# Kernel optimization log

Hardware: AMD Instinct MI355X
Metric: run time of the kernel (lower is better)

The kernel has to match this reference:

```python
import jax, jax.numpy as jnp
import numpy as np
import math

B, L, S, D = 4, 4096, 4096, 256
EPS = 1e-5

def _layernorm(x, g, b):
    mu = jnp.mean(x, axis=-1, keepdims=True)
    var = jnp.mean(jnp.square(x - mu), axis=-1, keepdims=True)
    return (x - mu) * jax.lax.rsqrt(var + EPS) * g + b

def setup_inputs() -> dict:
    key = jax.random.key(0)
    ks = jax.random.split(key, 14)
    s = 1.0 / math.sqrt(D)
    s2 = 1.0 / math.sqrt(2 * D)
    inp = {
        "source": jax.random.normal(ks[0], (B, L, D), jnp.float32),
        "target": jax.random.normal(ks[1], (B, S, D), jnp.float32),
        # linear weights stored as [in, out]
        "Wq": jax.random.uniform(ks[2], (D, D), jnp.float32, -s, s),
        "bq": jnp.zeros((D,), jnp.float32),
        "Wk": jax.random.uniform(ks[3], (D, D), jnp.float32, -s, s),
        "bk": jnp.zeros((D,), jnp.float32),
        "Wv": jax.random.uniform(ks[4], (D, D), jnp.float32, -s, s),
        "bv": jnp.zeros((D,), jnp.float32),
        "Wm": jax.random.uniform(ks[5], (D, D), jnp.float32, -s, s),
        "bm": jnp.zeros((D,), jnp.float32),
        "g1": jnp.ones((D,), jnp.float32),
        "beta1": jnp.zeros((D,), jnp.float32),
        "W1": jax.random.uniform(ks[6], (2 * D, 2 * D), jnp.float32, -s2, s2),
        "W2": jax.random.uniform(ks[7], (2 * D, D), jnp.float32, -s2, s2),
        "g2": jnp.ones((D,), jnp.float32),
        "beta2": jnp.zeros((D,), jnp.float32),
    }
    return inp

def reference(source, target, Wq, bq, Wk, bk, Wv, bv, Wm, bm, g1, beta1, W1, W2, g2, beta2):
    q = source @ Wq + bq              # [B, L, D]
    k = target @ Wk + bk              # [B, S, D]
    v = target @ Wv + bv              # [B, S, D]
    scale = 1.0 / math.sqrt(D)
    scores = jnp.einsum("bld,bsd->bls", q, k) * scale   # [B, L, S] materialized, as in source
    attn = jax.nn.softmax(scores, axis=-1)
    message = jnp.einsum("bls,bsd->bld", attn, v)        # [B, L, D]
    message = message @ Wm + bm
    message = _layernorm(message, g1, beta1)
    h = jnp.concatenate([source, message], axis=-1)      # [B, L, 2D]
    h = jax.nn.gelu(h @ W1, approximate=False)           # torch GELU is exact erf
    message = _layernorm(h @ W2, g2, beta2)
    return source + message
```

## Files before the change

### kernel.cpp

```cpp
#include <hip/hip_runtime.h>

typedef __bf16 bf16x8 __attribute__((ext_vector_type(8)));
typedef float f32x16 __attribute__((ext_vector_type(16)));
typedef float f32x4 __attribute__((ext_vector_type(4)));
typedef unsigned int u32;
typedef unsigned int u32x4 __attribute__((ext_vector_type(4)));
typedef unsigned short u16;
typedef unsigned short u16x4 __attribute__((ext_vector_type(4)));
typedef unsigned short u16x8 __attribute__((ext_vector_type(8)));

#define DEV static __device__ __forceinline__
#define AS1 __attribute__((address_space(1)))
#define AS3 __attribute__((address_space(3)))

DEV u16 f2bf(float f){
  unsigned u = __float_as_uint(f);
  u += 0x7FFFu + ((u >> 16) & 1u);
  return (u16)(u >> 16);
}
DEV float bf2f(u16 h){ return __uint_as_float(((u32)h) << 16); }

DEV void stage16(const u16* gsrc, const u16* ldst){
  __builtin_amdgcn_global_load_lds((const AS1 u32*)(unsigned long long)gsrc,
                                   (AS3 u32*)(u32)(unsigned long long)ldst,
                                   16, 0, 0);
}

constexpr int BATCH = 4, LQ = 4096, SK = 4096, DH = 256, BL = BATCH * LQ;
constexpr int NHALF = 2;
constexpr int ITERS = SK / NHALF / 64;

__global__ void prep_weights(const float* __restrict__ Wq, const float* __restrict__ Wk,
                             const float* __restrict__ Wv, const float* __restrict__ Wm,
                             const float* __restrict__ W1, const float* __restrict__ W2,
                             const float* __restrict__ bk, const float* __restrict__ bv,
                             u16* __restrict__ WqT, u16* __restrict__ WkvT,
                             u16* __restrict__ WmT,
                             u16* __restrict__ W1T, u16* __restrict__ W2T,
                             float* __restrict__ bkv){
  int idx = blockIdx.x * 256 + threadIdx.x;
  if (idx < 262144){
    int which = idx >> 16, i2 = idx & 65535;
    int r = i2 >> 8, c = i2 & 255;
    const float* S = (which==0)?Wq:(which==1)?Wk:(which==2)?Wv:Wm;
    u16*         D = (which==0)?WqT:(which==1)?WkvT:(which==2)?(WkvT+65536):WmT;
    D[c*256 + r] = f2bf(S[i2]);
  } else if (idx < 524288){
    int i2 = idx - 262144;
    int r = i2 >> 9, c = i2 & 511;
    W1T[c*512 + r] = f2bf(W1[i2]);
  } else if (idx < 655360){
    int i2 = idx - 524288;
    int r = i2 >> 8, c = i2 & 255;
    W2T[(size_t)c*512 + r] = f2bf(W2[i2]);
  } else if (idx < 655872){
    int i2 = idx - 655360;
    bkv[i2] = (i2 < 256) ? bk[i2] : bv[i2 - 256];
  }
}

__global__ __launch_bounds__(512, 2) void qkv_gemm(
  const float* __restrict__ src, const float* __restrict__ tgt,
  const u16* __restrict__ WqT, const u16* __restrict__ WkvT,
  const float* __restrict__ bq, const float* __restrict__ bkv,
  u16* __restrict__ qbuf, u16* __restrict__ kbuf, u16* __restrict__ vtbuf,
  u16* __restrict__ hcat, float qscale)
{
  __shared__ u16 A_lds[64 * 64];
  __shared__ u16 B_lds[256 * 64];
  const int tid = threadIdx.x, lane = tid & 63, wid = tid >> 6;
  const int ql = lane & 31, g = lane >> 5;
  const int path = blockIdx.x;
  const int m0 = blockIdx.y * 64;
  const float* Af = (path == 0) ? src : tgt;
  const u16* BTp = (path == 0) ? WqT : (WkvT + (size_t)(path - 1) * 65536);
  const float* bias = (path == 0) ? bq : (bkv + (path - 1) * 256);
  const int ar = tid >> 3, ac = (tid & 7) * 8;

  f32x16 acc[2] = {};
  f32x4 af0, af1;
  u32x4 breg[4];

#define QKV_LOAD_A(kb) do { \
    af0 = *(const f32x4*)&Af[(size_t)(m0+ar)*256 + (kb)*64 + ac]; \
    af1 = *(const f32x4*)&Af[(size_t)(m0+ar)*256 + (kb)*64 + ac + 4]; \
  } while(0)
#define QKV_LOAD_B(kb) do { \
    _Pragma("unroll") \
    for (int i = 0; i < 4; i++){ int item = tid + i*512; int r = item>>3, c = (item&7)*8; \
      breg[i] = *(const u32x4*)&BTp[(size_t)r*256 + (kb)*64 + c]; } \
  } while(0)

  QKV_LOAD_A(0); QKV_LOAD_B(0);

  for (int kb = 0; kb < 4; ++kb){
    __syncthreads();
    { u16x8 h;
      h[0]=f2bf(af0[0]); h[1]=f2bf(af0[1]); h[2]=f2bf(af0[2]); h[3]=f2bf(af0[3]);
      h[4]=f2bf(af1[0]); h[5]=f2bf(af1[1]); h[6]=f2bf(af1[2]); h[7]=f2bf(af1[3]);
      *(u16x8*)&A_lds[ar*64 + (ac ^ ((ar&7)*8))] = h;
      if (path == 0) *(u16x8*)&hcat[(size_t)(m0+ar)*512 + kb*64 + ac] = h;
    }
    #pragma unroll
    for (int i = 0; i < 4; i++){ int item = tid + i*512; int r = item>>3, c = (item&7)*8;
      *(u32x4*)&B_lds[r*64 + (c ^ ((r&7)*8))] = breg[i]; }
    __syncthreads();
    if (kb + 1 < 4){ QKV_LOAD_A(kb+1); QKV_LOAD_B(kb+1); }

    #pragma unroll
    for (int kk = 0; kk < 4; kk++){
      bf16x8 af[2];
      #pragma unroll
      for (int mi = 0; mi < 2; mi++)
        af[mi] = __builtin_bit_cast(bf16x8,
          *(const u32x4*)&A_lds[(mi*32+ql)*64 + ((kk*16+g*8) ^ ((ql&7)*8))]);
      bf16x8 bf = __builtin_bit_cast(bf16x8,
        *(const u32x4*)&B_lds[(wid*32+ql)*64 + ((kk*16+g*8) ^ ((ql&7)*8))]);
      #pragma unroll
      for (int mi = 0; mi < 2; mi++)
        acc[mi] = __builtin_amdgcn_mfma_f32_32x32x16_bf16(af[mi], bf, acc[mi], 0, 0, 0);
    }
  }

  const int col = wid*32 + ql;
  const float bv = bias[col];
  if (path == 2){
    #pragma unroll
    for (int mi = 0; mi < 2; mi++)
      #pragma unroll
      for (int qd = 0; qd < 4; qd++){
        u16x4 h;
        #pragma unroll
        for (int i = 0; i < 4; i++) h[i] = f2bf(acc[mi][qd*4+i] + bv);
        int row0 = m0 + mi*32 + qd*8 + 4*g;
        int bb = row0 >> 12, ss = row0 & 4095;
        *(u16x4*)&vtbuf[((size_t)bb*DH + col)*SK + ss] = h;
      }
  } else {
    u16* outp = (path == 0) ? qbuf : kbuf;
    const float sc = (path == 0) ? qscale : 1.0f;
    #pragma unroll
    for (int mi = 0; mi < 2; mi++)
      #pragma unroll
      for (int j = 0; j < 16; j++){
        int row = m0 + mi*32 + (j&3) + 8*(j>>2) + 4*g;
        outp[(size_t)row*256 + col] = f2bf((acc[mi][j] + bv) * sc);
      }
  }
}

__global__ __launch_bounds__(512, 2) void gemm_ln_wm(
  const u16* __restrict__ opart, const float* __restrict__ stats,
  const u16* __restrict__ BTp, const float* __restrict__ bias,
  const float* __restrict__ gamma, const float* __restrict__ beta,
  u16* __restrict__ outp)
{
  __shared__ __align__(16) char smem[65792];
  u16* A_lds = (u16*)smem;
  u16* B_lds = (u16*)(smem + 8192);
  float* scratch = (float*)smem;

  const int tid = threadIdx.x, lane = tid & 63, wid = tid >> 6;
  const int ql = lane & 31, g = lane >> 5;
  const int m0 = blockIdx.x * 64;
  const int ar = tid >> 3, ac = (tid & 7) * 8;

  float winv;
  { int row = m0 + ar;
    winv = 1.f / (stats[row] + stats[(size_t)BL + row]); }

  f32x16 acc[2] = {};
  u32x4 areg, areg2;
  u32x4 breg[4];

#define WM_LOAD_A(kb) do { \
    areg  = *(const u32x4*)&opart[(size_t)(m0+ar)*DH + (kb)*64 + ac]; \
    areg2 = *(const u32x4*)&opart[(size_t)BL*DH + (size_t)(m0+ar)*DH + (kb)*64 + ac]; \
  } while(0)
#define WM_LOAD_B(kb) do { \
    _Pragma("unroll") \
    for (int i = 0; i < 4; i++){ int item = tid + i*512; int r = item>>3, c = (item&7)*8; \
      breg[i] = *(const u32x4*)&BTp[(size_t)r*256 + (kb)*64 + c]; } \
  } while(0)

  WM_LOAD_A(0); WM_LOAD_B(0);

  for (int kb = 0; kb < 4; ++kb){
    __syncthreads();
    { u16x8 h;
      #pragma unroll
      for (int e = 0; e < 8; e++){
        u16 h0 = (u16)(areg[e>>1]  >> ((e&1)*16));
        u16 h1 = (u16)(areg2[e>>1] >> ((e&1)*16));
        h[e] = f2bf((bf2f(h0) + bf2f(h1)) * winv);
      }
      *(u16x8*)&A_lds[ar*64 + (ac ^ ((ar&7)*8))] = h; }
    #pragma unroll
    for (int i = 0; i < 4; i++){ int item = tid + i*512; int r = item>>3, c = (item&7)*8;
      *(u32x4*)&B_lds[r*64 + (c ^ ((r&7)*8))] = breg[i]; }
    __syncthreads();
    if (kb + 1 < 4){ WM_LOAD_A(kb+1); WM_LOAD_B(kb+1); }

    #pragma unroll
    for (int kk = 0; kk < 4; kk++){
      bf16x8 af[2];
      #pragma unroll
      for (int mi = 0; mi < 2; mi++)
        af[mi] = __builtin_bit_cast(bf16x8,
          *(const u32x4*)&A_lds[(mi*32+ql)*64 + ((kk*16+g*8) ^ ((ql&7)*8))]);
      bf16x8 bf = __builtin_bit_cast(bf16x8,
        *(const u32x4*)&B_lds[(wid*32+ql)*64 + ((kk*16+g*8) ^ ((ql&7)*8))]);
      #pragma unroll
      for (int mi = 0; mi < 2; mi++)
        acc[mi] = __builtin_amdgcn_mfma_f32_32x32x16_bf16(af[mi], bf, acc[mi], 0, 0, 0);
    }
  }

  __syncthreads();

  const float bv = bias[wid*32 + ql];
  #pragma unroll
  for (int mi = 0; mi < 2; mi++)
    #pragma unroll
    for (int j = 0; j < 16; j++){
      int row = mi*32 + (j&3) + 8*(j>>2) + 4*g;
      scratch[row*257 + wid*32 + ql] = acc[mi][j] + bv;
    }
  __syncthreads();

  f32x4 gv = *(const f32x4*)&gamma[lane*4];
  f32x4 bvv = *(const f32x4*)&beta[lane*4];
  #pragma unroll
  for (int rr = 0; rr < 8; rr++){
    const int row = wid*8 + rr;
    f32x4 v = *(const f32x4*)&scratch[row*257 + lane*4];
    float s1 = v[0]+v[1]+v[2]+v[3];
    float s2 = v[0]*v[0]+v[1]*v[1]+v[2]*v[2]+v[3]*v[3];
    #pragma unroll
    for (int m = 1; m < 64; m <<= 1){ s1 += __shfl_xor(s1, m, 64); s2 += __shfl_xor(s2, m, 64); }
    float mu = s1 * (1.f/DH);
    float var = s2 * (1.f/DH) - mu*mu;
    float rstd = rsqrtf(var + 1e-5f);
    u16x4 h;
    #pragma unroll
    for (int i = 0; i < 4; i++) h[i] = f2bf((v[i]-mu)*rstd*gv[i] + bvv[i]);
    *(u16x4*)&outp[(size_t)(m0+row)*512 + 256 + lane*4] = h;
  }
}

__global__ __launch_bounds__(512, 2) void fused_mlp(
  const u16* __restrict__ hcat, const u16* __restrict__ W1T,
  const u16* __restrict__ W2T, const float* __restrict__ gamma,
  const float* __restrict__ beta, const float* __restrict__ src,
  float* __restrict__ outp)
{
  __shared__ __align__(16) char smem[98304];
  u16* A1 = (u16*)smem;
  u16* B1 = (u16*)(smem + 8192);
  u16* Hl = (u16*)smem;
  u16* B2 = (u16*)(smem + 65536);
  float* scratch = (float*)smem;

  const int tid = threadIdx.x, lane = tid & 63, wid = tid >> 6;
  const int ql = lane & 31, g = lane >> 5;
  const int m0 = blockIdx.x * 64;

  f32x16 acc1[2][2] = {};
  for (int kb = 0; kb < 8; ++kb){
    if (kb) __syncthreads();
    { int r = tid >> 3, slot = tid & 7;
      stage16(&hcat[(size_t)(m0+r)*512 + kb*64 + ((slot ^ (r&7))<<3)],
              &A1[tid*8]); }
    #pragma unroll
    for (int i = 0; i < 8; i++){
      int grp = tid + i*512; int r = grp>>3, slot = grp&7;
      stage16(&W1T[(size_t)r*512 + kb*64 + ((slot ^ (r&7))<<3)], &B1[grp*8]);
    }
    __syncthreads();
    #pragma unroll
    for (int kk = 0; kk < 4; kk++){
      bf16x8 af[2];
      #pragma unroll
      for (int mi = 0; mi < 2; mi++)
        af[mi] = __builtin_bit_cast(bf16x8,
          *(const u32x4*)&A1[(mi*32+ql)*64 + ((kk*16+g*8) ^ ((ql&7)*8))]);
      #pragma unroll
      for (int ni = 0; ni < 2; ni++){
        int rB = wid*64 + ni*32 + ql;
        bf16x8 bf = __builtin_bit_cast(bf16x8,
          *(const u32x4*)&B1[rB*64 + ((kk*16+g*8) ^ ((ql&7)*8))]);
        #pragma unroll
        for (int mi = 0; mi < 2; mi++)
          acc1[mi][ni] = __builtin_amdgcn_mfma_f32_32x32x16_bf16(af[mi], bf, acc1[mi][ni], 0, 0, 0);
      }
    }
  }
  __syncthreads();

  #pragma unroll
  for (int mi = 0; mi < 2; mi++)
    #pragma unroll
    for (int ni = 0; ni < 2; ni++){
      const int col = wid*64 + ni*32 + ql;
      const int s = col >> 3;
      #pragma unroll
      for (int j = 0; j < 16; j++){
        int row = mi*32 + (j&3) + 8*(j>>2) + 4*g;
        float v = acc1[mi][ni][j];
        v = 0.5f * v * (1.f + erff(v * 0.70710678118f));
        Hl[row*512 + ((s ^ (row&7))<<3) + (col&7)] = f2bf(v);
      }
    }
  __syncthreads();

  f32x16 acc2[2] = {};
  for (int kb = 0; kb < 8; ++kb){
    if (kb) __syncthreads();
    #pragma unroll
    for (int i = 0; i < 4; i++){
      int grp = tid + i*512; int r = grp>>3, slot = grp&7;
      stage16(&W2T[(size_t)r*512 + kb*64 + ((slot ^ (r&7))<<3)], &B2[grp*8]);
    }
    __syncthreads();
    #pragma unroll
    for (int kk = 0; kk < 4; kk++){
      int c0s = (kb*64 + kk*16 + g*8) >> 3;
      bf16x8 af[2];
      #pragma unroll
      for (int mi = 0; mi < 2; mi++){
        int row = mi*32 + ql;
        af[mi] = __builtin_bit_cast(bf16x8,
          *(const u32x4*)&Hl[row*512 + ((c0s ^ (row&7))<<3)]);
      }
      bf16x8 bf = __builtin_bit_cast(bf16x8,
        *(const u32x4*)&B2[(wid*32+ql)*64 + ((kk*16+g*8) ^ ((ql&7)*8))]);
      #pragma unroll
      for (int mi = 0; mi < 2; mi++)
        acc2[mi] = __builtin_amdgcn_mfma_f32_32x32x16_bf16(af[mi], bf, acc2[mi], 0, 0, 0);
    }
  }
  __syncthreads();

  #pragma unroll
  for (int mi = 0; mi < 2; mi++)
    #pragma unroll
    for (int j = 0; j < 16; j++){
      int row = mi*32 + (j&3) + 8*(j>>2) + 4*g;
      scratch[row*257 + wid*32 + ql] = acc2[mi][j];
    }
  __syncthreads();

  f32x4 gv = *(const f32x4*)&gamma[lane*4];
  f32x4 bvv = *(const f32x4*)&beta[lane*4];
  #pragma unroll
  for (int rr = 0; rr < 8; rr++){
    const int row = wid*8 + rr;
    f32x4 v = *(const f32x4*)&scratch[row*257 + lane*4];
    float s1 = v[0]+v[1]+v[2]+v[3];
    float s2 = v[0]*v[0]+v[1]*v[1]+v[2]*v[2]+v[3]*v[3];
    #pragma unroll
    for (int m = 1; m < 64; m <<= 1){ s1 += __shfl_xor(s1, m, 64); s2 += __shfl_xor(s2, m, 64); }
    float mu = s1 * (1.f/DH);
    float var = s2 * (1.f/DH) - mu*mu;
    float rstd = rsqrtf(var + 1e-5f);
    f32x4 s = *(const f32x4*)&src[(size_t)(m0+row)*DH + lane*4];
    f32x4 o;
    #pragma unroll
    for (int i = 0; i < 4; i++) o[i] = s[i] + (v[i]-mu)*rstd*gv[i] + bvv[i];
    *(f32x4*)&outp[(size_t)(m0+row)*DH + lane*4] = o;
  }
}

__global__ __launch_bounds__(512, 2) void attn_kernel(
  const u16* __restrict__ qb, const u16* __restrict__ kb,
  const u16* __restrict__ vtb, u16* __restrict__ opart, float* __restrict__ stats)
{
  __shared__ u16 K_lds[2][64 * 256];
  __shared__ u16 VT_lds[2][256 * 64];
  __shared__ u32x4 P_exch[4][4][64];
  __shared__ float L_exch[4][2][32];

  const int tid = threadIdx.x;
  const int wid = tid >> 6, lane = tid & 63;
  const int ql = lane & 31, g = lane >> 5;
  const int qpair = wid >> 1, sh = wid & 1;
  const int b = blockIdx.y, half = blockIdx.z;
  const int qrow0 = blockIdx.x * 128 + qpair * 32;
  const int s0base = half * (SK / NHALF);

  const u16* kbase = kb  + (size_t)b * SK * DH;
  const u16* vbase = vtb + (size_t)b * DH * SK;

#define STAGE_K(bi, s0) do { \
    _Pragma("unroll") \
    for (int i = 0; i < 4; i++){ \
      int grp = tid + i*512; int s = grp>>5, slot = grp&31; \
      stage16(kbase + (size_t)((s0)+s)*DH + ((slot ^ (s&31))<<3), \
              &K_lds[bi][(i*512 + wid*64)*8]); \
    } } while(0)
#define STAGE_V(bi, s0) do { \
    _Pragma("unroll") \
    for (int i = 0; i < 4; i++){ \
      int grp = tid + i*512; int d = grp>>3, slot = grp&7; \
      stage16(vbase + (size_t)d*SK + (s0) + ((slot ^ (d&7))<<3), \
              &VT_lds[bi][(i*512 + wid*64)*8]); \
    } } while(0)

  STAGE_K(0, s0base);
  STAGE_V(0, s0base);

  bf16x8 qf[16];
  {
    const u16* qp = qb + ((size_t)(b*LQ + qrow0 + ql)) * DH + g * 8;
    #pragma unroll
    for (int kk = 0; kk < 16; kk++)
      qf[kk] = __builtin_bit_cast(bf16x8, *(const u32x4*)(qp + kk*16));
  }

  f32x16 accO[4] = {};
  float l_lane = 0.f;

  __syncthreads();

  for (int it = 0; it < ITERS; ++it){
    const int cur = it & 1;
    if (it + 1 < ITERS){
      STAGE_K(cur ^ 1, s0base + (it+1)*64);
      STAGE_V(cur ^ 1, s0base + (it+1)*64);
    }

    f32x16 ps = {};
    __builtin_amdgcn_s_setprio(1);
    #pragma unroll
    for (int kk = 0; kk < 16; ++kk){
      bf16x8 kf = __builtin_bit_cast(bf16x8,
        *(const u32x4*)&K_lds[cur][(sh*32+ql)*256 + (((kk*2+g) ^ ql)<<3)]);
      ps = __builtin_amdgcn_mfma_f32_32x32x16_bf16(kf, qf[kk], ps, 0, 0, 0);
    }
    __builtin_amdgcn_s_setprio(0);

    #pragma unroll
    for (int j = 0; j < 16; j++) ps[j] = exp2f(ps[j]);

    u32 Wp[4][2];
    #pragma unroll
    for (int qd = 0; qd < 4; qd++)
      #pragma unroll
      for (int h = 0; h < 2; h++){
        float lo = ps[qd*4 + 2*h], hi = ps[qd*4 + 2*h + 1];
        asm("v_cvt_pk_bf16_f32 %0, %1, %2" : "=v"(Wp[qd][h]) : "v"(lo), "v"(hi));
      }
    bf16x8 pfo[2];
    #pragma unroll
    for (int i = 0; i < 2; i++){
      const int qp2 = i * 2;
      u32 a0 = Wp[qp2][0], b0 = Wp[qp2+1][0];
      u32 a1 = Wp[qp2][1], b1 = Wp[qp2+1][1];
      asm("v_permlane32_swap_b32 %0, %1" : "+v"(a0), "+v"(b0));
      asm("v_permlane32_swap_b32 %0, %1" : "+v"(a1), "+v"(b1));
      u32x4 w; w[0] = a0; w[1] = a1; w[2] = b0; w[3] = b1;
      P_exch[qpair][sh*2 + i][lane] = w;
      pfo[i] = __builtin_bit_cast(bf16x8, w);
    }

    __builtin_amdgcn_s_setprio(1);
    #pragma unroll
    for (int dt = 0; dt < 4; dt++){
      const int dtg = sh*4 + dt;
      const int k0 = sh*2;
      bf16x8 vf0 = __builtin_bit_cast(bf16x8,
        *(const u32x4*)&VT_lds[cur][(dtg*32+ql)*64 + ((((k0+0)*2+g) ^ (ql&7))<<3)]);
      accO[dt] = __builtin_amdgcn_mfma_f32_32x32x16_bf16(vf0, pfo[0], accO[dt], 0, 0, 0);
      bf16x8 vf1 = __builtin_bit_cast(bf16x8,
        *(const u32x4*)&VT_lds[cur][(dtg*32+ql)*64 + ((((k0+1)*2+g) ^ (ql&7))<<3)]);
      accO[dt] = __builtin_amdgcn_mfma_f32_32x32x16_bf16(vf1, pfo[1], accO[dt], 0, 0, 0);
    }
    __builtin_amdgcn_s_setprio(0);

    { float s8[8];
      #pragma unroll
      for (int j = 0; j < 8; j++) s8[j] = ps[j] + ps[j+8];
      l_lane += ((s8[0]+s8[4]) + (s8[1]+s8[5])) + ((s8[2]+s8[6]) + (s8[3]+s8[7])); }

    asm volatile("s_waitcnt lgkmcnt(0)" ::: "memory");
    __builtin_amdgcn_s_barrier();
    __builtin_amdgcn_sched_barrier(0);

    bf16x8 pfp0 = __builtin_bit_cast(bf16x8, P_exch[qpair][(sh^1)*2 + 0][lane]);
    bf16x8 pfp1 = __builtin_bit_cast(bf16x8, P_exch[qpair][(sh^1)*2 + 1][lane]);

    __builtin_amdgcn_s_setprio(1);
    #pragma unroll
    for (int dt = 0; dt < 4; dt++){
      const int dtg = sh*4 + dt;
      const int k0 = (sh^1)*2;
      bf16x8 vf0 = __builtin_bit_cast(bf16x8,
        *(const u32x4*)&VT_lds[cur][(dtg*32+ql)*64 + ((((k0+0)*2+g) ^ (ql&7))<<3)]);
      accO[dt] = __builtin_amdgcn_mfma_f32_32x32x16_bf16(vf0, pfp0, accO[dt], 0, 0, 0);
      bf16x8 vf1 = __builtin_bit_cast(bf16x8,
        *(const u32x4*)&VT_lds[cur][(dtg*32+ql)*64 + ((((k0+1)*2+g) ^ (ql&7))<<3)]);
      accO[dt] = __builtin_amdgcn_mfma_f32_32x32x16_bf16(vf1, pfp1, accO[dt], 0, 0, 0);
    }
    __builtin_amdgcn_s_setprio(0);

    asm volatile("s_waitcnt vmcnt(0) lgkmcnt(0)" ::: "memory");
    __builtin_amdgcn_s_barrier();
    __builtin_amdgcn_sched_barrier(0);
  }

  float l_run = l_lane + __shfl_xor(l_lane, 32, 64);
  if (g == 0) L_exch[qpair][sh][ql] = l_run;
  __syncthreads();
  float l_tot = l_run + L_exch[qpair][sh^1][ql];

  const int rowb = b * LQ + qrow0;
  if (sh == 0 && g == 0)
    stats[(size_t)half*BL + rowb + ql] = l_tot;

  float* scratch = (float*)&K_lds[0][0] + wid * 1056;
  #pragma unroll
  for (int dt = 0; dt < 4; dt++){
    const int dtg = sh*4 + dt;
    #pragma unroll
    for (int j = 0; j < 16; j++){
      int dl = (j&3) + 8*(j>>2) + 4*g;
      scratch[ql*33 + dl] = accO[dt][j];
    }
    int q2 = lane >> 1, dl2 = (lane & 1) * 16;
    u16x8 h0, h1;
    #pragma unroll
    for (int i = 0; i < 8; i++){ h0[i] = f2bf(scratch[q2*33 + dl2 + i]);
                                 h1[i] = f2bf(scratch[q2*33 + dl2 + 8 + i]); }
    u16* op = &opart[((size_t)half*BL + rowb + q2)*DH + dtg*32 + dl2];
    *(u16x8*)op = h0;
    *(u16x8*)(op + 8) = h1;
  }
}

extern "C" void kernel_launch(void* const* d_in, const int* in_sizes, int n_in,
                              void* d_out, int out_size, void* d_ws, size_t ws_size,
                              hipStream_t stream)
{
  const float* source = (const float*)d_in[0];
  const float* target = (const float*)d_in[1];
  const float* Wq = (const float*)d_in[2];  const float* bq = (const float*)d_in[3];
  const float* Wk = (const float*)d_in[4];  const float* bk = (const float*)d_in[5];
  const float* Wv = (const float*)d_in[6];  const float* bv = (const float*)d_in[7];
  const float* Wm = (const float*)d_in[8];  const float* bm = (const float*)d_in[9];
  const float* g1 = (const float*)d_in[10]; const float* be1 = (const float*)d_in[11];
  const float* W1 = (const float*)d_in[12]; const float* W2 = (const float*)d_in[13];
  const float* g2 = (const float*)d_in[14]; const float* be2 = (const float*)d_in[15];

  char* ws = (char*)d_ws;
  u16* WqT  = (u16*)(ws);
  u16* WkvT = (u16*)(ws + (size_t)(1u<<17));
  u16* WmT  = (u16*)(ws + (size_t)3*(1u<<17));
  u16* W1T  = (u16*)(ws + (size_t)4*(1u<<17));
  u16* W2T  = (u16*)(ws + (size_t)8*(1u<<17));
  float* bkv = (float*)(ws + (size_t)10*(1u<<17));
  size_t off = (size_t)10*(1u<<17) + 4096;
  u16* qbuf  = (u16*)(ws + off); off += (size_t)BL*DH*2;
  u16* kbuf  = (u16*)(ws + off); off += (size_t)BL*DH*2;
  u16* vtbuf = (u16*)(ws + off); off += (size_t)BL*DH*2;
  u16* hcat  = (u16*)(ws + off); off += (size_t)BL*512*2;
  u16* opart = (u16*)(ws + off); off += (size_t)NHALF*BL*DH*2;
  float* stats = (float*)(ws + off); off += (size_t)NHALF*BL*4;

  prep_weights<<<dim3(2562), 256, 0, stream>>>(Wq, Wk, Wv, Wm, W1, W2, bk, bv,
                                               WqT, WkvT, WmT, W1T, W2T, bkv);

  const float qscale = 1.4426950408889634f / 16.0f;
  qkv_gemm<<<dim3(3, BL/64), 512, 0, stream>>>(
      source, target, WqT, WkvT, bq, bkv, qbuf, kbuf, vtbuf, hcat, qscale);

  attn_kernel<<<dim3(LQ/128, BATCH, NHALF), 512, 0, stream>>>(qbuf, kbuf, vtbuf, opart, stats);

  gemm_ln_wm<<<dim3(BL/64), 512, 0, stream>>>(opart, stats, WmT, bm, g1, be1, hcat);

  fused_mlp<<<dim3(BL/64), 512, 0, stream>>>(hcat, W1T, W2T, g2, be2, source,
                                             (float*)d_out);
}
```

Before: 153.0 us.

## Fuse Wm projection+LayerNorm with MLP kernel, keeping concat tile in LDS

Merges the Wm GEMM/LayerNorm kernel and the MLP kernel into one kernel that builds the [source, message] bf16 tile in shared memory, converting source directly from fp32. This removes the global hcat buffer, its writes from the QKV kernel and its reads in the MLP, plus one kernel launch. It raises shared memory per block to about 128 KB, which limits residency to one block per CU.

```diff
diff --git a/kernel.cpp b/kernel.cpp
--- a/kernel.cpp
+++ b/kernel.cpp
@@ -64,7 +64,7 @@
   const u16* __restrict__ WqT, const u16* __restrict__ WkvT,
   const float* __restrict__ bq, const float* __restrict__ bkv,
   u16* __restrict__ qbuf, u16* __restrict__ kbuf, u16* __restrict__ vtbuf,
-  u16* __restrict__ hcat, float qscale)
+  float qscale)
 {
   __shared__ u16 A_lds[64 * 64];
   __shared__ u16 B_lds[256 * 64];
@@ -99,7 +99,6 @@
       h[0]=f2bf(af0[0]); h[1]=f2bf(af0[1]); h[2]=f2bf(af0[2]); h[3]=f2bf(af0[3]);
       h[4]=f2bf(af1[0]); h[5]=f2bf(af1[1]); h[6]=f2bf(af1[2]); h[7]=f2bf(af1[3]);
       *(u16x8*)&A_lds[ar*64 + (ac ^ ((ar&7)*8))] = h;
-      if (path == 0) *(u16x8*)&hcat[(size_t)(m0+ar)*512 + kb*64 + ac] = h;
     }
     #pragma unroll
     for (int i = 0; i < 4; i++){ int item = tid + i*512; int r = item>>3, c = (item&7)*8;
@@ -149,21 +148,40 @@
   }
 }
 
-__global__ __launch_bounds__(512, 2) void gemm_ln_wm(
+__global__ __launch_bounds__(512, 2) void wm_mlp(
   const u16* __restrict__ opart, const float* __restrict__ stats,
-  const u16* __restrict__ BTp, const float* __restrict__ bias,
-  const float* __restrict__ gamma, const float* __restrict__ beta,
-  u16* __restrict__ outp)
+  const u16* __restrict__ WmT, const float* __restrict__ bm,
+  const float* __restrict__ g1, const float* __restrict__ be1,
+  const u16* __restrict__ W1T, const u16* __restrict__ W2T,
+  const float* __restrict__ g2, const float* __restrict__ be2,
+  const float* __restrict__ src, float* __restrict__ outp)
 {
-  __shared__ __align__(16) char smem[65792];
-  u16* A_lds = (u16*)smem;
-  u16* B_lds = (u16*)(smem + 8192);
-  float* scratch = (float*)smem;
+  __shared__ __align__(16) char smem[131328];
+  u16* Hc = (u16*)smem;
+  char* rb = smem + 65536;
+  u16* A_lds = (u16*)rb;
+  u16* B_lds = (u16*)(rb + 8192);
+  float* scr = (float*)rb;
+  u16* B1 = (u16*)rb;
+  u16* B2 = (u16*)rb;
 
   const int tid = threadIdx.x, lane = tid & 63, wid = tid >> 6;
   const int ql = lane & 31, g = lane >> 5;
   const int m0 = blockIdx.x * 64;
   const int ar = tid >> 3, ac = (tid & 7) * 8;
+
+  #pragma unroll
+  for (int i = 0; i < 4; i++){
+    int idx = tid + i*512;
+    int r = idx >> 5, c8 = (idx & 31) * 8;
+    f32x4 a = *(const f32x4*)&src[(size_t)(m0+r)*256 + c8];
+    f32x4 b = *(const f32x4*)&src[(size_t)(m0+r)*256 + c8 + 4];
+    u16x8 h;
+    h[0]=f2bf(a[0]); h[1]=f2bf(a[1]); h[2]=f2bf(a[2]); h[3]=f2bf(a[3]);
+    h[4]=f2bf(b[0]); h[5]=f2bf(b[1]); h[6]=f2bf(b[2]); h[7]=f2bf(b[3]);
+    int s = c8 >> 3;
+    *(u16x8*)&Hc[r*512 + ((s ^ (r&7))<<3)] = h;
+  }
 
   float winv;
   { int row = m0 + ar;
@@ -180,9 +198,10 @@
 #define WM_LOAD_B(kb) do { \
     _Pragma("unroll") \
     for (int i = 0; i < 4; i++){ int item = tid + i*512; int r = item>>3, c = (item&7)*8; \
-      breg[i] = *(const u32x4*)&BTp[(size_t)r*256 + (kb)*64 + c]; } \
+      breg[i] = *(const u32x4*)&BTpWm[(size_t)r*256 + (kb)*64 + c]; } \
   } while(0)
 
+  const u16* BTpWm = WmT;
   WM_LOAD_A(0); WM_LOAD_B(0);
 
   for (int kb = 0; kb < 4; ++kb){
@@ -218,59 +237,43 @@
 
   __syncthreads();
 
-  const float bv = bias[wid*32 + ql];
-  #pragma unroll
-  for (int mi = 0; mi < 2; mi++)
-    #pragma unroll
-    for (int j = 0; j < 16; j++){
-      int row = mi*32 + (j&3) + 8*(j>>2) + 4*g;
-      scratch[row*257 + wid*32 + ql] = acc[mi][j] + bv;
-    }
-  __syncthreads();
-
-  f32x4 gv = *(const f32x4*)&gamma[lane*4];
-  f32x4 bvv = *(const f32x4*)&beta[lane*4];
-  #pragma unroll
-  for (int rr = 0; rr < 8; rr++){
-    const int row = wid*8 + rr;
-    f32x4 v = *(const f32x4*)&scratch[row*257 + lane*4];
-    float s1 = v[0]+v[1]+v[2]+v[3];
-    float s2 = v[0]*v[0]+v[1]*v[1]+v[2]*v[2]+v[3]*v[3];
-    #pragma unroll
-    for (int m = 1; m < 64; m <<= 1){ s1 += __shfl_xor(s1, m, 64); s2 += __shfl_xor(s2, m, 64); }
-    float mu = s1 * (1.f/DH);
-    float var = s2 * (1.f/DH) - mu*mu;
-    float rstd = rsqrtf(var + 1e-5f);
-    u16x4 h;
-    #pragma unroll
-    for (int i = 0; i < 4; i++) h[i] = f2bf((v[i]-mu)*rstd*gv[i] + bvv[i]);
-    *(u16x4*)&outp[(size_t)(m0+row)*512 + 256 + lane*4] = h;
-  }
-}
-
-__global__ __launch_bounds__(512, 2) void fused_mlp(
-  const u16* __restrict__ hcat, const u16* __restrict__ W1T,
-  const u16* __restrict__ W2T, const float* __restrict__ gamma,
-  const float* __restrict__ beta, const float* __restrict__ src,
-  float* __restrict__ outp)
-{
-  __shared__ __align__(16) char smem[98304];
-  u16* A1 = (u16*)smem;
-  u16* B1 = (u16*)(smem + 8192);
-  u16* Hl = (u16*)smem;
-  u16* B2 = (u16*)(smem + 65536);
-  float* scratch = (float*)smem;
-
-  const int tid = threadIdx.x, lane = tid & 63, wid = tid >> 6;
-  const int ql = lane & 31, g = lane >> 5;
-  const int m0 = blockIdx.x * 64;
+  { const float bv = bm[wid*32 + ql];
+    #pragma unroll
+    for (int mi = 0; mi < 2; mi++)
+      #pragma unroll
+      for (int j = 0; j < 16; j++){
+        int row = mi*32 + (j&3) + 8*(j>>2) + 4*g;
+        scr[row*257 + wid*32 + ql] = acc[mi][j] + bv;
+      }
+  }
+  __syncthreads();
+
+  { f32x4 gv = *(const f32x4*)&g1[lane*4];
+    f32x4 bvv = *(const f32x4*)&be1[lane*4];
+    #pragma unroll
+    for (int rr = 0; rr < 8; rr++){
+      const int row = wid*8 + rr;
+      f32x4 v = *(const f32x4*)&scr[row*257 + lane*4];
+      float s1 = v[0]+v[1]+v[2]+v[3];
+      float s2 = v[0]*v[0]+v[1]*v[1]+v[2]*v[2]+v[3]*v[3];
+      #pragma unroll
+      for (int m = 1; m < 64; m <<= 1){ s1 += __shfl_xor(s1, m, 64); s2 += __shfl_xor(s2, m, 64); }
+      float mu = s1 * (1.f/DH);
+      float var = s2 * (1.f/DH) - mu*mu;
+      float rstd = rsqrtf(var + 1e-5f);
+      u16x4 h;
+      #pragma unroll
+      for (int i = 0; i < 4; i++) h[i] = f2bf((v[i]-mu)*rstd*gv[i] + bvv[i]);
+      const int col = 256 + lane*4;
+      const int s = col >> 3;
+      *(u16x4*)&Hc[row*512 + ((s ^ (row&7))<<3) + (col & 7)] = h;
+    }
+  }
+  __syncthreads();
 
   f32x16 acc1[2][2] = {};
   for (int kb = 0; kb < 8; ++kb){
     if (kb) __syncthreads();
-    { int r = tid >> 3, slot = tid & 7;
-      stage16(&hcat[(size_t)(m0+r)*512 + kb*64 + ((slot ^ (r&7))<<3)],
-              &A1[tid*8]); }
     #pragma unroll
     for (int i = 0; i < 8; i++){
       int grp = tid + i*512; int r = grp>>3, slot = grp&7;
@@ -279,11 +282,14 @@
     __syncthreads();
     #pragma unroll
     for (int kk = 0; kk < 4; kk++){
+      const int c0s = (kb*64 + kk*16 + g*8) >> 3;
       bf16x8 af[2];
       #pragma unroll
-      for (int mi = 0; mi < 2; mi++)
+      for (int mi = 0; mi < 2; mi++){
+        int row = mi*32 + ql;
         af[mi] = __builtin_bit_cast(bf16x8,
-          *(const u32x4*)&A1[(mi*32+ql)*64 + ((kk*16+g*8) ^ ((ql&7)*8))]);
+          *(const u32x4*)&Hc[row*512 + ((c0s ^ (row&7))<<3)]);
+      }
       #pragma unroll
       for (int ni = 0; ni < 2; ni++){
         int rB = wid*64 + ni*32 + ql;
@@ -308,7 +314,7 @@
         int row = mi*32 + (j&3) + 8*(j>>2) + 4*g;
         float v = acc1[mi][ni][j];
         v = 0.5f * v * (1.f + erff(v * 0.70710678118f));
-        Hl[row*512 + ((s ^ (row&7))<<3) + (col&7)] = f2bf(v);
+        Hc[row*512 + ((s ^ (row&7))<<3) + (col&7)] = f2bf(v);
       }
     }
   __syncthreads();
@@ -324,13 +330,13 @@
     __syncthreads();
     #pragma unroll
     for (int kk = 0; kk < 4; kk++){
-      int c0s = (kb*64 + kk*16 + g*8) >> 3;
+      const int c0s = (kb*64 + kk*16 + g*8) >> 3;
       bf16x8 af[2];
       #pragma unroll
       for (int mi = 0; mi < 2; mi++){
         int row = mi*32 + ql;
         af[mi] = __builtin_bit_cast(bf16x8,
-          *(const u32x4*)&Hl[row*512 + ((c0s ^ (row&7))<<3)]);
+          *(const u32x4*)&Hc[row*512 + ((c0s ^ (row&7))<<3)]);
       }
       bf16x8 bf = __builtin_bit_cast(bf16x8,
         *(const u32x4*)&B2[(wid*32+ql)*64 + ((kk*16+g*8) ^ ((ql&7)*8))]);
@@ -346,28 +352,29 @@
     #pragma unroll
     for (int j = 0; j < 16; j++){
       int row = mi*32 + (j&3) + 8*(j>>2) + 4*g;
-      scratch[row*257 + wid*32 + ql] = acc2[mi][j];
-    }
-  __syncthreads();
-
-  f32x4 gv = *(const f32x4*)&gamma[lane*4];
-  f32x4 bvv = *(const f32x4*)&beta[lane*4];
-  #pragma unroll
-  for (int rr = 0; rr < 8; rr++){
-    const int row = wid*8 + rr;
-    f32x4 v = *(const f32x4*)&scratch[row*257 + lane*4];
-    float s1 = v[0]+v[1]+v[2]+v[3];
-    float s2 = v[0]*v[0]+v[1]*v[1]+v[2]*v[2]+v[3]*v[3];
-    #pragma unroll
-    for (int m = 1; m < 64; m <<= 1){ s1 += __shfl_xor(s1, m, 64); s2 += __shfl_xor(s2, m, 64); }
-    float mu = s1 * (1.f/DH);
-    float var = s2 * (1.f/DH) - mu*mu;
-    float rstd = rsqrtf(var + 1e-5f);
-    f32x4 s = *(const f32x4*)&src[(size_t)(m0+row)*DH + lane*4];
-    f32x4 o;
-    #pragma unroll
-    for (int i = 0; i < 4; i++) o[i] = s[i] + (v[i]-mu)*rstd*gv[i] + bvv[i];
-    *(f32x4*)&outp[(size_t)(m0+row)*DH + lane*4] = o;
+      scr[row*257 + wid*32 + ql] = acc2[mi][j];
+    }
+  __syncthreads();
+
+  { f32x4 gv = *(const f32x4*)&g2[lane*4];
+    f32x4 bvv = *(const f32x4*)&be2[lane*4];
+    #pragma unroll
+    for (int rr = 0; rr < 8; rr++){
+      const int row = wid*8 + rr;
+      f32x4 v = *(const f32x4*)&scr[row*257 + lane*4];
+      float s1 = v[0]+v[1]+v[2]+v[3];
+      float s2 = v[0]*v[0]+v[1]*v[1]+v[2]*v[2]+v[3]*v[3];
+      #pragma unroll
+      for (int m = 1; m < 64; m <<= 1){ s1 += __shfl_xor(s1, m, 64); s2 += __shfl_xor(s2, m, 64); }
+      float mu = s1 * (1.f/DH);
+      float var = s2 * (1.f/DH) - mu*mu;
+      float rstd = rsqrtf(var + 1e-5f);
+      f32x4 s = *(const f32x4*)&src[(size_t)(m0+row)*DH + lane*4];
+      f32x4 o;
+      #pragma unroll
+      for (int i = 0; i < 4; i++) o[i] = s[i] + (v[i]-mu)*rstd*gv[i] + bvv[i];
+      *(f32x4*)&outp[(size_t)(m0+row)*DH + lane*4] = o;
+    }
   }
 }
 
@@ -562,7 +569,6 @@
   u16* qbuf  = (u16*)(ws + off); off += (size_t)BL*DH*2;
   u16* kbuf  = (u16*)(ws + off); off += (size_t)BL*DH*2;
   u16* vtbuf = (u16*)(ws + off); off += (size_t)BL*DH*2;
-  u16* hcat  = (u16*)(ws + off); off += (size_t)BL*512*2;
   u16* opart = (u16*)(ws + off); off += (size_t)NHALF*BL*DH*2;
   float* stats = (float*)(ws + off); off += (size_t)NHALF*BL*4;
 
@@ -571,12 +577,11 @@
 
   const float qscale = 1.4426950408889634f / 16.0f;
   qkv_gemm<<<dim3(3, BL/64), 512, 0, stream>>>(
-      source, target, WqT, WkvT, bq, bkv, qbuf, kbuf, vtbuf, hcat, qscale);
+      source, target, WqT, WkvT, bq, bkv, qbuf, kbuf, vtbuf, qscale);
 
   attn_kernel<<<dim3(LQ/128, BATCH, NHALF), 512, 0, stream>>>(qbuf, kbuf, vtbuf, opart, stats);
 
-  gemm_ln_wm<<<dim3(BL/64), 512, 0, stream>>>(opart, stats, WmT, bm, g1, be1, hcat);
-
-  fused_mlp<<<dim3(BL/64), 512, 0, stream>>>(hcat, W1T, W2T, g2, be2, source,
-                                             (float*)d_out);
-}
+  wm_mlp<<<dim3(BL/64), 512, 0, stream>>>(opart, stats, WmT, bm, g1, be1,
+                                          W1T, W2T, g2, be2, source,
+                                          (float*)d_out);
+}
```

Measured after the change: 151.6 us. No clear change (-0.9%).
